# Kernel optimization log

Measured on AMD Instinct MI355X. Metric: run time of the kernel, lower is better.

Reference implementation:

```python
import jax, jax.numpy as jnp
import numpy as np

N_SAMPLES = 8_388_608   # total packed samples (~64 per ray on average)
N_RAYS = 131_072
DT_SCALE = 0.005        # keep per-ray optical depth ~O(1); also tempers global-cumsum fp32 error


def setup_inputs() -> dict:
    key = jax.random.key(0)
    k1, k2, k3, k4, k5 = jax.random.split(key, 5)
    rgb_samples = jax.random.uniform(k1, (N_SAMPLES, 3), dtype=jnp.float32)
    radiance_samples = jax.random.uniform(k2, (N_SAMPLES, 1), dtype=jnp.float32)  # density sigma >= 0
    samples_z = jax.random.uniform(k3, (N_SAMPLES,), dtype=jnp.float32)           # t values in [0,1)
    samples_dt = jax.random.uniform(k4, (N_SAMPLES,), dtype=jnp.float32) * DT_SCALE
    # sorted segment ids == contiguous packed per-ray sample ranges (ragged)
    ray_id = jnp.sort(jax.random.randint(k5, (N_SAMPLES,), 0, N_RAYS, dtype=jnp.int64))
    ray_t_exit = jnp.full((N_RAYS, 1), 2.0, dtype=jnp.float32)  # exit t beyond all z -> positive last dt
    return {
        "rgb_samples": rgb_samples,
        "radiance_samples": radiance_samples,
        "samples_z": samples_z,
        "samples_dt": samples_dt,
        "ray_id": ray_id,
        "ray_t_exit": ray_t_exit,
        "use_ray_t_exit": 1,
    }


def reference(rgb_samples, radiance_samples, samples_z, samples_dt, ray_id, ray_t_exit, use_ray_t_exit):
    N = rgb_samples.shape[0]
    sigma = radiance_samples[:, 0]
    idx = jnp.arange(N)

    # dt of the last sample of each ray is (t_exit - z_last) when use_ray_t_exit
    if use_ray_t_exit:
        last_idx = jax.ops.segment_max(idx, ray_id, num_segments=N_RAYS)
        is_last = idx == last_idx[ray_id]
        dt = jnp.where(is_last, ray_t_exit[ray_id, 0] - samples_z, samples_dt)
    else:
        dt = samples_dt

    sigdt = sigma * dt                      # optical depth per sample
    c = jnp.cumsum(sigdt)                   # global inclusive cumsum
    c_excl = c - sigdt                      # global exclusive cumsum
    # exclusive cumsum restarted per ray: subtract value at each segment's first sample
    # (c_excl is non-decreasing since sigdt >= 0, so segment_min == first element)
    seg_start = jax.ops.segment_min(c_excl, ray_id, num_segments=N_RAYS)
    T = jnp.exp(-(c_excl - seg_start[ray_id]))          # transmittance before each sample
    alpha = 1.0 - jnp.exp(-sigdt)
    w = alpha * T                                        # per-sample compositing weight

    pred_rgb = jax.ops.segment_sum(w[:, None] * rgb_samples, ray_id, num_segments=N_RAYS)   # [R,3]
    pred_depth = jax.ops.segment_sum(w * samples_z, ray_id, num_segments=N_RAYS)[:, None]   # [R,1]
    bg_transmittance = jnp.exp(-jax.ops.segment_sum(sigdt, ray_id, num_segments=N_RAYS))[:, None]  # [R,1]
    weight_per_sample = w[:, None]                                                           # [N,1]
    return pred_rgb, pred_depth, bg_transmittance, weight_per_sample
```

## Files before the change

### kernel.cpp

```cpp
#include <hip/hip_runtime.h>


#define RPW 4

template <int CTRL, int ROW_MASK>
__device__ __forceinline__ float dpp_add(float x) {
    int t = __builtin_amdgcn_update_dpp(0, __float_as_int(x), CTRL, ROW_MASK, 0xf, true);
    return x + __int_as_float(t);
}

__device__ __forceinline__ float wave_incl_scan(float x) {
    x = dpp_add<0x111, 0xf>(x);
    x = dpp_add<0x112, 0xf>(x);
    x = dpp_add<0x114, 0xf>(x);
    x = dpp_add<0x118, 0xf>(x);
    x = dpp_add<0x142, 0xa>(x);
    x = dpp_add<0x143, 0xc>(x);
    return x;
}

__device__ __forceinline__ float readlane_f32(float x, int lane) {
    return __int_as_float(__builtin_amdgcn_readlane(__float_as_int(x), lane));
}

__global__ void compute_starts_kernel(const int* __restrict__ ray_id,
                                      int n_samples, int n_rays,
                                      int* __restrict__ starts) {
    const int t = blockIdx.x * blockDim.x + threadIdx.x;
    const int stride = gridDim.x * blockDim.x;
    if (t == 0) {
        const int first = ray_id[0];
        for (int r = 0; r <= first; ++r) starts[r] = 0;
        const int last = ray_id[n_samples - 1];
        for (int r = last + 1; r <= n_rays; ++r) starts[r] = n_samples;
    }
    for (int g = t; g * 4 < n_samples; g += stride) {
        const int i4 = g * 4;
        const int4 v = *reinterpret_cast<const int4*>(ray_id + i4);
        const int prev = (i4 == 0) ? v.x : ray_id[i4 - 1];
        const int vals[5] = {prev, v.x, v.y, v.z, v.w};
        #pragma unroll
        for (int j = 0; j < 4; ++j) {
            const int p = vals[j], c = vals[j + 1];
            if (c != p) {
                for (int r = p + 1; r <= c; ++r) starts[r] = i4 + j;
            }
        }
    }
}

__device__ __forceinline__ void process_chunk(
    float sg, float zv, float dtv, float cr, float cg, float cb,
    int base, int s1, int lane, int use_exit, float texit,
    float& csum, float& accR, float& accG, float& accB, float& accD,
    float* __restrict__ out_w)
{
    const int i = base + lane;
    const bool active = i < s1;
    if (use_exit && i == s1 - 1) dtv = texit - zv;
    const float sigdt = active ? sg * dtv : 0.f;
    const float scan  = wave_incl_scan(sigdt);
    const float cexcl = csum + (scan - sigdt);
    const float T     = __expf(-cexcl);
    const float alpha = 1.f - __expf(-sigdt);
    const float w     = alpha * T;
    if (active) out_w[i] = w;
    accR += w * cr;
    accG += w * cg;
    accB += w * cb;
    accD += w * zv;
    csum += readlane_f32(scan, 63);
}

__global__ __launch_bounds__(256) void render_kernel(
    const float* __restrict__ rgb,
    const float* __restrict__ sigma_in,
    const float* __restrict__ z_in,
    const float* __restrict__ dt_in,
    const float* __restrict__ t_exit,
    const int*  __restrict__ use_exit_p,
    const int*  __restrict__ starts,
    float* __restrict__ out_rgb,
    float* __restrict__ out_depth,
    float* __restrict__ out_bg,
    float* __restrict__ out_w,
    int n_rays, int n_samples)
{
    const int wave = threadIdx.x >> 6;
    const int lane = threadIdx.x & 63;
    const int wid  = blockIdx.x * (blockDim.x >> 6) + wave;
    const int ray0 = wid * RPW;
    if (ray0 >= n_rays) return;

    int s[RPW + 1];
    #pragma unroll
    for (int k = 0; k <= RPW; ++k) {
        s[k] = starts[min(ray0 + k, n_rays)];
    }
    const int use_exit = *use_exit_p;
    float texit[RPW];
    #pragma unroll
    for (int k = 0; k < RPW; ++k) {
        texit[k] = t_exit[min(ray0 + k, n_rays - 1)];
    }

    float sg1[RPW], z1[RPW], dt1[RPW], cr1[RPW], cg1[RPW], cb1[RPW];
    float sg2[RPW], z2[RPW], dt2[RPW], cr2[RPW], cg2[RPW], cb2[RPW];
    const int imax = n_samples - 1;
    #pragma unroll
    for (int k = 0; k < RPW; ++k) {
        const int i1 = min(s[k] + lane, imax);
        sg1[k] = sigma_in[i1];
        z1[k]  = z_in[i1];
        dt1[k] = dt_in[i1];
        cr1[k] = rgb[3 * i1 + 0];
        cg1[k] = rgb[3 * i1 + 1];
        cb1[k] = rgb[3 * i1 + 2];
    }
    #pragma unroll
    for (int k = 0; k < RPW; ++k) {
        const int i2 = min(s[k] + 64 + lane, imax);
        sg2[k] = sigma_in[i2];
        z2[k]  = z_in[i2];
        dt2[k] = dt_in[i2];
        cr2[k] = rgb[3 * i2 + 0];
        cg2[k] = rgb[3 * i2 + 1];
        cb2[k] = rgb[3 * i2 + 2];
    }

    #pragma unroll
    for (int k = 0; k < RPW; ++k) {
        const int ray = ray0 + k;
        if (ray >= n_rays) break;
        const int s0 = s[k], s1 = s[k + 1];
        float csum = 0.f, accR = 0.f, accG = 0.f, accB = 0.f, accD = 0.f;

        process_chunk(sg1[k], z1[k], dt1[k], cr1[k], cg1[k], cb1[k],
                      s0, s1, lane, use_exit, texit[k],
                      csum, accR, accG, accB, accD, out_w);
        if (s0 + 64 < s1) {
            process_chunk(sg2[k], z2[k], dt2[k], cr2[k], cg2[k], cb2[k],
                          s0 + 64, s1, lane, use_exit, texit[k],
                          csum, accR, accG, accB, accD, out_w);
        }
        for (int base = s0 + 128; base < s1; base += 64) {
            const int i = min(base + lane, imax);
            const float sg = sigma_in[i];
            const float zv = z_in[i];
            const float dtv = dt_in[i];
            const float cr = rgb[3 * i + 0];
            const float cg = rgb[3 * i + 1];
            const float cb = rgb[3 * i + 2];
            process_chunk(sg, zv, dtv, cr, cg, cb,
                          base, s1, lane, use_exit, texit[k],
                          csum, accR, accG, accB, accD, out_w);
        }

        accR = wave_incl_scan(accR);
        accG = wave_incl_scan(accG);
        accB = wave_incl_scan(accB);
        accD = wave_incl_scan(accD);
        if (lane == 63) {
            out_rgb[3 * ray + 0] = accR;
            out_rgb[3 * ray + 1] = accG;
            out_rgb[3 * ray + 2] = accB;
            out_depth[ray] = accD;
            out_bg[ray]    = __expf(-csum);
        }
    }
}

extern "C" void kernel_launch(void* const* d_in, const int* in_sizes, int n_in,
                              void* d_out, int out_size, void* d_ws, size_t ws_size,
                              hipStream_t stream) {
    const float* rgb     = (const float*)d_in[0];
    const float* sigma   = (const float*)d_in[1];
    const float* z       = (const float*)d_in[2];
    const float* dt      = (const float*)d_in[3];
    const int*   ray_id  = (const int*)d_in[4];
    const float* t_exit  = (const float*)d_in[5];
    const int*   use_ex  = (const int*)d_in[6];

    const int n_samples = in_sizes[2];
    const int n_rays    = in_sizes[5];

    int* starts = (int*)d_ws;

    float* out      = (float*)d_out;
    float* out_rgb  = out;
    float* out_dep  = out + (size_t)3 * n_rays;
    float* out_bg   = out + (size_t)4 * n_rays;
    float* out_w    = out + (size_t)5 * n_rays;

    compute_starts_kernel<<<2048, 256, 0, stream>>>(ray_id, n_samples, n_rays, starts);

    const int waves_per_block = 4;
    const int rays_per_block  = waves_per_block * RPW;
    const int blocks = (n_rays + rays_per_block - 1) / rays_per_block;
    render_kernel<<<blocks, 256, 0, stream>>>(rgb, sigma, z, dt, t_exit, use_ex,
                                              starts, out_rgb, out_dep, out_bg,
                                              out_w, n_rays, n_samples);
}
```

Baseline: 52.82 us.

## Compute weights as transmittance differences and skip unneeded second-chunk loads

Computes each weight as T_prev - T, using one exp per sample and a wave-shift DPP with a carried value, replacing the previous two exps. The background transmittance is taken from the carried T instead of a separate exp. The second 64-sample prefetch now runs only for rays that need it, and uniform values are forced into scalar registers with readfirstlane. Taking the difference of exponentials can lose fp32 precision for small weights. The row_shr DPP (0x138) is assumed to cross rows on wave64, which holds on CDNA.

```diff
diff --git a/kernel.cpp b/kernel.cpp
--- a/kernel.cpp
+++ b/kernel.cpp
@@ -2,6 +2,8 @@
 
 
 #define RPW 4
+
+struct F3 { float x, y, z; };
 
 template <int CTRL, int ROW_MASK>
 __device__ __forceinline__ float dpp_add(float x) {
@@ -49,27 +51,29 @@
     }
 }
 
-__device__ __forceinline__ void process_chunk(
-    float sg, float zv, float dtv, float cr, float cg, float cb,
+__device__ __forceinline__ void process_chunk64(
+    float sg, float zv, float dtv, F3 c,
     int base, int s1, int lane, int use_exit, float texit,
-    float& csum, float& accR, float& accG, float& accB, float& accD,
+    float& csum, float& carry,
+    float& accR, float& accG, float& accB, float& accD,
     float* __restrict__ out_w)
 {
     const int i = base + lane;
     const bool active = i < s1;
     if (use_exit && i == s1 - 1) dtv = texit - zv;
     const float sigdt = active ? sg * dtv : 0.f;
-    const float scan  = wave_incl_scan(sigdt);
-    const float cexcl = csum + (scan - sigdt);
-    const float T     = __expf(-cexcl);
-    const float alpha = 1.f - __expf(-sigdt);
-    const float w     = alpha * T;
+    const float t = csum + wave_incl_scan(sigdt);
+    const float v = __expf(-t);
+    const int vp = __builtin_amdgcn_update_dpp(__float_as_int(carry), __float_as_int(v),
+                                               0x138 , 0xf, 0xf, false);
+    const float w = __int_as_float(vp) - v;
     if (active) out_w[i] = w;
-    accR += w * cr;
-    accG += w * cg;
-    accB += w * cb;
+    accR += w * c.x;
+    accG += w * c.y;
+    accB += w * c.z;
     accD += w * zv;
-    csum += readlane_f32(scan, 63);
+    csum  = readlane_f32(t, 63);
+    carry = readlane_f32(v, 63);
 }
 
 __global__ __launch_bounds__(256) void render_kernel(
@@ -92,68 +96,72 @@
     const int ray0 = wid * RPW;
     if (ray0 >= n_rays) return;
 
+    const int use_exit = *use_exit_p;
+    const int imax = n_samples - 1;
+
     int s[RPW + 1];
     #pragma unroll
     for (int k = 0; k <= RPW; ++k) {
-        s[k] = starts[min(ray0 + k, n_rays)];
-    }
-    const int use_exit = *use_exit_p;
+        s[k] = __builtin_amdgcn_readfirstlane(starts[min(ray0 + k, n_rays)]);
+    }
     float texit[RPW];
     #pragma unroll
     for (int k = 0; k < RPW; ++k) {
-        texit[k] = t_exit[min(ray0 + k, n_rays - 1)];
-    }
-
-    float sg1[RPW], z1[RPW], dt1[RPW], cr1[RPW], cg1[RPW], cb1[RPW];
-    float sg2[RPW], z2[RPW], dt2[RPW], cr2[RPW], cg2[RPW], cb2[RPW];
-    const int imax = n_samples - 1;
+        texit[k] = readlane_f32(t_exit[min(ray0 + k, n_rays - 1)], 0);
+    }
+
+    float sg1[RPW], z1[RPW], dt1[RPW];
+    F3 c1[RPW];
     #pragma unroll
     for (int k = 0; k < RPW; ++k) {
         const int i1 = min(s[k] + lane, imax);
         sg1[k] = sigma_in[i1];
         z1[k]  = z_in[i1];
         dt1[k] = dt_in[i1];
-        cr1[k] = rgb[3 * i1 + 0];
-        cg1[k] = rgb[3 * i1 + 1];
-        cb1[k] = rgb[3 * i1 + 2];
-    }
-    #pragma unroll
-    for (int k = 0; k < RPW; ++k) {
-        const int i2 = min(s[k] + 64 + lane, imax);
-        sg2[k] = sigma_in[i2];
-        z2[k]  = z_in[i2];
-        dt2[k] = dt_in[i2];
-        cr2[k] = rgb[3 * i2 + 0];
-        cg2[k] = rgb[3 * i2 + 1];
-        cb2[k] = rgb[3 * i2 + 2];
-    }
+        c1[k]  = *reinterpret_cast<const F3*>(rgb + 3 * (size_t)i1);
+    }
+
+    float sg2[RPW], z2[RPW], dt2[RPW];
+    F3 c2[RPW];
+    bool need2[RPW];
+    #pragma unroll
+    for (int k = 0; k < RPW; ++k) {
+        need2[k] = (s[k] + 64) < s[k + 1];
+        if (need2[k]) {
+            const int i2 = min(s[k] + 64 + lane, imax);
+            sg2[k] = sigma_in[i2];
+            z2[k]  = z_in[i2];
+            dt2[k] = dt_in[i2];
+            c2[k]  = *reinterpret_cast<const F3*>(rgb + 3 * (size_t)i2);
+        }
+    }
+    __builtin_amdgcn_sched_barrier(0);
 
     #pragma unroll
     for (int k = 0; k < RPW; ++k) {
         const int ray = ray0 + k;
         if (ray >= n_rays) break;
         const int s0 = s[k], s1 = s[k + 1];
-        float csum = 0.f, accR = 0.f, accG = 0.f, accB = 0.f, accD = 0.f;
-
-        process_chunk(sg1[k], z1[k], dt1[k], cr1[k], cg1[k], cb1[k],
-                      s0, s1, lane, use_exit, texit[k],
-                      csum, accR, accG, accB, accD, out_w);
-        if (s0 + 64 < s1) {
-            process_chunk(sg2[k], z2[k], dt2[k], cr2[k], cg2[k], cb2[k],
-                          s0 + 64, s1, lane, use_exit, texit[k],
-                          csum, accR, accG, accB, accD, out_w);
+        float csum = 0.f, carry = 1.0f;
+        float accR = 0.f, accG = 0.f, accB = 0.f, accD = 0.f;
+
+        process_chunk64(sg1[k], z1[k], dt1[k], c1[k],
+                        s0, s1, lane, use_exit, texit[k],
+                        csum, carry, accR, accG, accB, accD, out_w);
+        if (need2[k]) {
+            process_chunk64(sg2[k], z2[k], dt2[k], c2[k],
+                            s0 + 64, s1, lane, use_exit, texit[k],
+                            csum, carry, accR, accG, accB, accD, out_w);
         }
         for (int base = s0 + 128; base < s1; base += 64) {
             const int i = min(base + lane, imax);
             const float sg = sigma_in[i];
             const float zv = z_in[i];
             const float dtv = dt_in[i];
-            const float cr = rgb[3 * i + 0];
-            const float cg = rgb[3 * i + 1];
-            const float cb = rgb[3 * i + 2];
-            process_chunk(sg, zv, dtv, cr, cg, cb,
-                          base, s1, lane, use_exit, texit[k],
-                          csum, accR, accG, accB, accD, out_w);
+            const F3 cc = *reinterpret_cast<const F3*>(rgb + 3 * (size_t)i);
+            process_chunk64(sg, zv, dtv, cc,
+                            base, s1, lane, use_exit, texit[k],
+                            csum, carry, accR, accG, accB, accD, out_w);
         }
 
         accR = wave_incl_scan(accR);
@@ -165,7 +173,7 @@
             out_rgb[3 * ray + 1] = accG;
             out_rgb[3 * ray + 2] = accB;
             out_depth[ray] = accD;
-            out_bg[ray]    = __expf(-csum);
+            out_bg[ray]    = carry;
         }
     }
 }
```

Result: no change. 52.91 us (+0.2%).
